# Performance work log

Hardware: AMD Instinct MI355X
Metric: run time of the kernel (lower is better)

Reference implementation:

```python
import jax, jax.numpy as jnp
import numpy as np

B, S, D, N, C = 32, 1024, 256, 32, 64
ROUTING_ITERS = 3


def setup_inputs() -> dict:
    key = jax.random.key(0)
    k1, k2 = jax.random.split(key)
    x = jax.random.normal(k1, (B, S, D), dtype=jnp.float32)
    W = jax.random.normal(k2, (N, D, C), dtype=jnp.float32) * 0.1
    return {"x": x, "W": W}


def _squash(s, eps=1e-8):
    # s: [B, N, C]; squash along last dim
    sq_norm = jnp.sum(s * s, axis=-1, keepdims=True)
    return (sq_norm / (1.0 + sq_norm)) * s / jnp.sqrt(sq_norm + eps)


def reference(x, W):
    # Prediction vectors: u_hat[b,s,n,c] = sum_d x[b,s,d] * W[n,d,c]
    u_hat = jnp.einsum('bsd,ndc->bsnc', x, W)  # [B, S, N, C]
    b_logits = jnp.zeros(u_hat.shape[:3], dtype=u_hat.dtype)  # [B, S, N]
    v = None
    for i in range(ROUTING_ITERS):
        c = jax.nn.softmax(b_logits, axis=2)               # [B, S, N]
        s = jnp.einsum('bsn,bsnc->bnc', c, u_hat)          # [B, N, C]
        v = _squash(s)                                      # [B, N, C]
        if i < ROUTING_ITERS - 1:
            agreement = jnp.einsum('bsnc,bnc->bsn', u_hat, v)
            b_logits = b_logits + agreement
    return v
```

## Files before the change

### kernel.cpp

```cpp
#include <hip/hip_runtime.h>
#include <math.h>

namespace {
constexpr int B_ = 32, S_ = 1024, D_ = 256, N_ = 32, C_ = 64;
constexpr int NC_ = N_ * C_;
constexpr int XP_ = 16;

typedef __bf16 bf16x8 __attribute__((ext_vector_type(8)));
typedef __bf16 bf16x4 __attribute__((ext_vector_type(4)));
typedef float floatx4 __attribute__((ext_vector_type(4)));

constexpr int XS_ = 264;
constexpr int TS_ = 264;
constexpr int CS_ = 72;
}

extern "C" __global__ __launch_bounds__(256) void k_stage(
    const float* __restrict__ x, float* __restrict__ xsum_part,
    __bf16* __restrict__ xb_ws) {
  const int b = blockIdx.x, sb = blockIdx.y, t = threadIdx.x;
  const float* xb = x + ((size_t)b * S_ + sb * 64) * D_;
  float a = 0.f;
  #pragma unroll 8
  for (int s = 0; s < 64; ++s) a += xb[s * D_ + t];
  xsum_part[((size_t)b * XP_ + sb) * D_ + t] = a;

  __bf16* xo = xb_ws + ((size_t)(b * XP_ + sb)) * (64 * D_);
  #pragma unroll
  for (int i = 0; i < 16; ++i) {
    int pos = i * 1024 + t * 4;
    float4 f = *(const float4*)(xb + pos);
    bf16x4 p4;
    p4[0] = (__bf16)f.x; p4[1] = (__bf16)f.y;
    p4[2] = (__bf16)f.z; p4[3] = (__bf16)f.w;
    *(bf16x4*)(xo + pos) = p4;
  }
}

extern "C" __global__ __launch_bounds__(256) void k_small(
    const float* __restrict__ z, const float* __restrict__ W,
    float* __restrict__ t_fp, __bf16* __restrict__ t_bhi,
    __bf16* __restrict__ t_blo, float* __restrict__ vout,
    float* __restrict__ yzero,
    int P, int zb, int zp, int zn, float scale, int accum, int final_) {
  __shared__ float zloc[256];
  __shared__ float sq_red[4][64];
  __shared__ float v_lds[64];
  const int b = blockIdx.x, n = blockIdx.y, t = threadIdx.x;

  float a = 0.f;
  for (int p = 0; p < P; ++p) a += z[(size_t)b * zb + (size_t)p * zp + n * zn + t];
  zloc[t] = a;
  if (yzero) yzero[((size_t)b * N_ + n) * D_ + t] = 0.f;
  __syncthreads();

  const int c = t & 63, dq = t >> 6;
  const float* Wn = W + (size_t)n * (D_ * C_);
  float s = 0.f;
  #pragma unroll 8
  for (int dd = 0; dd < 64; ++dd) {
    int d = dq * 64 + dd;
    s += zloc[d] * Wn[d * 64 + c];
  }
  sq_red[dq][c] = s;
  __syncthreads();

  if (t < 64) {
    float sc = (sq_red[0][t] + sq_red[1][t] + sq_red[2][t] + sq_red[3][t]) * scale;
    float sq = sc * sc;
    #pragma unroll
    for (int m = 1; m <= 32; m <<= 1) sq += __shfl_xor(sq, m);
    float scl = sq / ((1.f + sq) * sqrtf(sq + 1e-8f));
    float v = sc * scl;
    v_lds[t] = v;
    if (final_) vout[(size_t)b * NC_ + n * 64 + t] = v;
  }
  __syncthreads();

  if (!final_) {
    const float4* W4 = (const float4*)Wn + t * 16;
    float acc = 0.f;
    #pragma unroll
    for (int q = 0; q < 16; ++q) {
      float4 wv = W4[q];
      acc += wv.x * v_lds[q * 4] + wv.y * v_lds[q * 4 + 1] +
             wv.z * v_lds[q * 4 + 2] + wv.w * v_lds[q * 4 + 3];
    }
    size_t idx = ((size_t)b * N_ + n) * D_ + t;
    float tf = acc + (accum ? t_fp[idx] : 0.f);
    t_fp[idx] = tf;
    __bf16 hi = (__bf16)tf;
    t_bhi[idx] = hi;
    t_blo[idx] = (__bf16)(tf - (float)hi);
  }
}

extern "C" __global__ __launch_bounds__(256) void k_pass(
    const __bf16* __restrict__ xb_ws, const __bf16* __restrict__ t_bhi,
    const __bf16* __restrict__ t_blo, float* __restrict__ y) {
  __shared__ __align__(16) __bf16 x_lds[64 * XS_];
  __shared__ __align__(16) __bf16 th_lds[N_ * TS_];
  __shared__ __align__(16) __bf16 tl_lds[N_ * TS_];
  __shared__ __align__(16) __bf16 c_Th[N_ * CS_];
  __shared__ __align__(16) __bf16 c_Tl[N_ * CS_];
  const int b = blockIdx.x, ch = blockIdx.y;
  const int t = threadIdx.x, w = t >> 6, lane = t & 63;
  const int quad = lane >> 4, l16 = lane & 15;

  #pragma unroll
  for (int e = 0; e < 4; ++e) {
    int idx = e * 2048 + t * 8;
    int n = idx >> 8, d = idx & 255;
    *(uint4*)(th_lds + n * TS_ + d) = *(const uint4*)(t_bhi + (size_t)b * 8192 + idx);
    *(uint4*)(tl_lds + n * TS_ + d) = *(const uint4*)(t_blo + (size_t)b * 8192 + idx);
  }
  const __bf16* xsrc = xb_ws + ((size_t)(b * XP_ + ch)) * (64 * D_);
  #pragma unroll
  for (int e = 0; e < 8; ++e) {
    int idx = e * 2048 + t * 8;
    int row = idx >> 8, col = idx & 255;
    *(uint4*)(x_lds + row * XS_ + col) = *(const uint4*)(xsrc + idx);
  }
  __syncthreads();

  floatx4 acc[2];
  acc[0] = (floatx4){0.f, 0.f, 0.f, 0.f};
  acc[1] = (floatx4){0.f, 0.f, 0.f, 0.f};
  const int sbase = w * 16;
  #pragma unroll
  for (int k0 = 0; k0 < 256; k0 += 32) {
    int ks = k0 + quad * 8;
    bf16x8 bfrag = *(const bf16x8*)(x_lds + (sbase + l16) * XS_ + ks);
    #pragma unroll
    for (int i = 0; i < 2; ++i) {
      bf16x8 ah = *(const bf16x8*)(th_lds + (i * 16 + l16) * TS_ + ks);
      bf16x8 al = *(const bf16x8*)(tl_lds + (i * 16 + l16) * TS_ + ks);
      acc[i] = __builtin_amdgcn_mfma_f32_16x16x32_bf16(ah, bfrag, acc[i], 0, 0, 0);
      acc[i] = __builtin_amdgcn_mfma_f32_16x16x32_bf16(al, bfrag, acc[i], 0, 0, 0);
    }
  }
  float mx = -1e30f;
  #pragma unroll
  for (int i = 0; i < 2; ++i)
    #pragma unroll
    for (int r = 0; r < 4; ++r) mx = fmaxf(mx, acc[i][r]);
  mx = fmaxf(mx, __shfl_xor(mx, 16));
  mx = fmaxf(mx, __shfl_xor(mx, 32));
  float e_[2][4];
  float ss = 0.f;
  #pragma unroll
  for (int i = 0; i < 2; ++i)
    #pragma unroll
    for (int r = 0; r < 4; ++r) { e_[i][r] = __expf(acc[i][r] - mx); ss += e_[i][r]; }
  ss += __shfl_xor(ss, 16);
  ss += __shfl_xor(ss, 32);
  float inv = 1.f / ss;
  #pragma unroll
  for (int i = 0; i < 2; ++i)
    #pragma unroll
    for (int r = 0; r < 4; ++r) {
      float cv = e_[i][r] * inv;
      __bf16 chi = (__bf16)cv;
      int o = (i * 16 + quad * 4 + r) * CS_ + sbase + l16;
      c_Th[o] = chi;
      c_Tl[o] = (__bf16)(cv - (float)chi);
    }
  __syncthreads();

  floatx4 acc2[2][4];
  #pragma unroll
  for (int i = 0; i < 2; ++i)
    #pragma unroll
    for (int dt = 0; dt < 4; ++dt) acc2[i][dt] = (floatx4){0.f, 0.f, 0.f, 0.f};
  const int dbase = w * 64;
  #pragma unroll
  for (int k0 = 0; k0 < 64; k0 += 32) {
    int ks = k0 + quad * 8;
    bf16x8 ah[2], al[2];
    #pragma unroll
    for (int i = 0; i < 2; ++i) {
      ah[i] = *(const bf16x8*)(c_Th + (i * 16 + l16) * CS_ + ks);
      al[i] = *(const bf16x8*)(c_Tl + (i * 16 + l16) * CS_ + ks);
    }
    #pragma unroll
    for (int dt = 0; dt < 4; ++dt) {
      bf16x8 bfr;
      #pragma unroll
      for (int j8 = 0; j8 < 8; ++j8)
        bfr[j8] = x_lds[(ks + j8) * XS_ + dbase + dt * 16 + l16];
      #pragma unroll
      for (int i = 0; i < 2; ++i) {
        acc2[i][dt] = __builtin_amdgcn_mfma_f32_16x16x32_bf16(ah[i], bfr, acc2[i][dt], 0, 0, 0);
        acc2[i][dt] = __builtin_amdgcn_mfma_f32_16x16x32_bf16(al[i], bfr, acc2[i][dt], 0, 0, 0);
      }
    }
  }
  #pragma unroll
  for (int i = 0; i < 2; ++i)
    #pragma unroll
    for (int dt = 0; dt < 4; ++dt)
      #pragma unroll
      for (int r = 0; r < 4; ++r) {
        int n = i * 16 + quad * 4 + r;
        int d = dbase + dt * 16 + l16;
        atomicAdd(&y[((size_t)b * N_ + n) * D_ + d], acc2[i][dt][r]);
      }
}

extern "C" void kernel_launch(void* const* d_in, const int* in_sizes, int n_in,
                              void* d_out, int out_size, void* d_ws, size_t ws_size,
                              hipStream_t stream) {
  const float* x = (const float*)d_in[0];
  const float* W = (const float*)d_in[1];
  float* out = (float*)d_out;

  char* ws = (char*)d_ws;
  __bf16* xb_ws = (__bf16*)ws;
  float* xsum_part = (float*)(ws + 16777216);
  float* y1 = (float*)(ws + 16777216 + 524288);
  float* y2 = y1 + B_ * N_ * D_;
  float* t_fp = y2 + B_ * N_ * D_;
  __bf16* t_bhi = (__bf16*)(t_fp + B_ * N_ * D_);
  __bf16* t_blo = t_bhi + B_ * N_ * D_;

  k_stage<<<dim3(B_, XP_), 256, 0, stream>>>(x, xsum_part, xb_ws);

  k_small<<<dim3(B_, N_), 256, 0, stream>>>(
      xsum_part, W, t_fp, t_bhi, t_blo, nullptr, y1,
      XP_, XP_ * D_, D_, 0, 1.f / 32.f, 0, 0);

  k_pass<<<dim3(B_, XP_), 256, 0, stream>>>(xb_ws, t_bhi, t_blo, y1);

  k_small<<<dim3(B_, N_), 256, 0, stream>>>(
      y1, W, t_fp, t_bhi, t_blo, nullptr, y2,
      1, N_ * D_, 0, D_, 1.f, 1, 0);

  k_pass<<<dim3(B_, XP_), 256, 0, stream>>>(xb_ws, t_bhi, t_blo, y2);

  k_small<<<dim3(B_, N_), 256, 0, stream>>>(
      y2, W, t_fp, t_bhi, t_blo, out, nullptr,
      1, N_ * D_, 0, D_, 1.f, 0, 1);
}
```

Baseline: 158.5 us.

## Fuse all routing stages into one persistent kernel with grid barriers

```diff
diff --git a/kernel.cpp b/kernel.cpp
--- a/kernel.cpp
+++ b/kernel.cpp
@@ -5,239 +5,281 @@
 constexpr int B_ = 32, S_ = 1024, D_ = 256, N_ = 32, C_ = 64;
 constexpr int NC_ = N_ * C_;
 constexpr int XP_ = 16;
+constexpr unsigned NBLK = B_ * XP_;
 
 typedef __bf16 bf16x8 __attribute__((ext_vector_type(8)));
 typedef __bf16 bf16x4 __attribute__((ext_vector_type(4)));
 typedef float floatx4 __attribute__((ext_vector_type(4)));
 
 constexpr int XS_ = 264;
-constexpr int TS_ = 264;
 constexpr int CS_ = 72;
 }
 
-extern "C" __global__ __launch_bounds__(256) void k_stage(
-    const float* __restrict__ x, float* __restrict__ xsum_part,
-    __bf16* __restrict__ xb_ws) {
-  const int b = blockIdx.x, sb = blockIdx.y, t = threadIdx.x;
-  const float* xb = x + ((size_t)b * S_ + sb * 64) * D_;
-  float a = 0.f;
-  #pragma unroll 8
-  for (int s = 0; s < 64; ++s) a += xb[s * D_ + t];
-  xsum_part[((size_t)b * XP_ + sb) * D_ + t] = a;
-
-  __bf16* xo = xb_ws + ((size_t)(b * XP_ + sb)) * (64 * D_);
-  #pragma unroll
-  for (int i = 0; i < 16; ++i) {
-    int pos = i * 1024 + t * 4;
-    float4 f = *(const float4*)(xb + pos);
-    bf16x4 p4;
-    p4[0] = (__bf16)f.x; p4[1] = (__bf16)f.y;
-    p4[2] = (__bf16)f.z; p4[3] = (__bf16)f.w;
-    *(bf16x4*)(xo + pos) = p4;
-  }
-}
-
-extern "C" __global__ __launch_bounds__(256) void k_small(
-    const float* __restrict__ z, const float* __restrict__ W,
-    float* __restrict__ t_fp, __bf16* __restrict__ t_bhi,
-    __bf16* __restrict__ t_blo, float* __restrict__ vout,
-    float* __restrict__ yzero,
-    int P, int zb, int zp, int zn, float scale, int accum, int final_) {
-  __shared__ float zloc[256];
+__device__ __forceinline__ void gsync(unsigned* cnt, unsigned* go, unsigned e,
+                                      int t) {
+  __syncthreads();
+  if (t == 0) {
+    __threadfence();
+    unsigned a = __hip_atomic_fetch_add(cnt, 1u, __ATOMIC_ACQ_REL,
+                                        __HIP_MEMORY_SCOPE_AGENT) + 1u;
+    if (a == e * NBLK) {
+      __hip_atomic_store(go, e, __ATOMIC_RELEASE, __HIP_MEMORY_SCOPE_AGENT);
+    } else {
+      while (__hip_atomic_load(go, __ATOMIC_ACQUIRE,
+                               __HIP_MEMORY_SCOPE_AGENT) < e) {
+        __builtin_amdgcn_s_sleep(32);
+      }
+    }
+    __threadfence();
+  }
+  __syncthreads();
+}
+
+extern "C" __global__ __launch_bounds__(256, 2) void k_fused(
+    const float* __restrict__ x, const float* __restrict__ W,
+    float* __restrict__ out, float* __restrict__ xsum_part,
+    float* __restrict__ y1, float* __restrict__ y2,
+    __bf16* __restrict__ t_bhi, __bf16* __restrict__ t_blo,
+    unsigned* bar_cnt, unsigned* bar_go) {
+  __shared__ __align__(16) __bf16 x_lds[64 * XS_];
+  __shared__ __align__(16) __bf16 c_Th[N_ * CS_];
+  __shared__ __align__(16) __bf16 c_Tl[N_ * CS_];
+  __shared__ __align__(16) float scr[1024];
   __shared__ float sq_red[4][64];
   __shared__ float v_lds[64];
-  const int b = blockIdx.x, n = blockIdx.y, t = threadIdx.x;
-
-  float a = 0.f;
-  for (int p = 0; p < P; ++p) a += z[(size_t)b * zb + (size_t)p * zp + n * zn + t];
-  zloc[t] = a;
-  if (yzero) yzero[((size_t)b * N_ + n) * D_ + t] = 0.f;
+
+  const int bid = blockIdx.x;
+  const int b = bid >> 4, ch = bid & 15;
+  const int t = threadIdx.x, w = t >> 6, lane = t & 63;
+  const int quad = lane >> 4, l16 = lane & 15;
+
+  {
+    const float* xb = x + ((size_t)b * S_ + ch * 64) * D_;
+    float s0 = 0.f, s1 = 0.f, s2 = 0.f, s3 = 0.f;
+#pragma unroll
+    for (int i = 0; i < 16; ++i) {
+      int pos = i * 1024 + t * 4;
+      int row = pos >> 8, col = pos & 255;
+      float4 f = *(const float4*)(xb + pos);
+      bf16x4 p4;
+      p4[0] = (__bf16)f.x; p4[1] = (__bf16)f.y;
+      p4[2] = (__bf16)f.z; p4[3] = (__bf16)f.w;
+      *(bf16x4*)(x_lds + row * XS_ + col) = p4;
+      s0 += f.x; s1 += f.y; s2 += f.z; s3 += f.w;
+    }
+    ((float4*)scr)[t] = make_float4(s0, s1, s2, s3);
+  }
   __syncthreads();
-
-  const int c = t & 63, dq = t >> 6;
-  const float* Wn = W + (size_t)n * (D_ * C_);
-  float s = 0.f;
-  #pragma unroll 8
-  for (int dd = 0; dd < 64; ++dd) {
-    int d = dq * 64 + dd;
-    s += zloc[d] * Wn[d * 64 + c];
-  }
-  sq_red[dq][c] = s;
-  __syncthreads();
-
   if (t < 64) {
-    float sc = (sq_red[0][t] + sq_red[1][t] + sq_red[2][t] + sq_red[3][t]) * scale;
-    float sq = sc * sc;
-    #pragma unroll
-    for (int m = 1; m <= 32; m <<= 1) sq += __shfl_xor(sq, m);
-    float scl = sq / ((1.f + sq) * sqrtf(sq + 1e-8f));
-    float v = sc * scl;
-    v_lds[t] = v;
-    if (final_) vout[(size_t)b * NC_ + n * 64 + t] = v;
-  }
-  __syncthreads();
-
-  if (!final_) {
+    float4 a0 = ((float4*)scr)[t], a1 = ((float4*)scr)[t + 64],
+           a2 = ((float4*)scr)[t + 128], a3 = ((float4*)scr)[t + 192];
+    float4 r;
+    r.x = a0.x + a1.x + a2.x + a3.x;
+    r.y = a0.y + a1.y + a2.y + a3.y;
+    r.z = a0.z + a1.z + a2.z + a3.z;
+    r.w = a0.w + a1.w + a2.w + a3.w;
+    *(float4*)(xsum_part + (size_t)bid * D_ + t * 4) = r;
+  }
+
+  auto small_sv = [&](const float* zsrc, int P, int zp, const float* Wn,
+                      float scale) {
+    __syncthreads();
+    float a = 0.f;
+    for (int p = 0; p < P; ++p) a += zsrc[(size_t)p * zp + t];
+    scr[t] = a;
+    __syncthreads();
+    const int c = t & 63, dq = t >> 6;
+    float s = 0.f;
+#pragma unroll 8
+    for (int dd = 0; dd < 64; ++dd) {
+      int d = dq * 64 + dd;
+      s += scr[d] * Wn[d * 64 + c];
+    }
+    sq_red[dq][c] = s;
+    __syncthreads();
+    if (t < 64) {
+      float sc =
+          (sq_red[0][t] + sq_red[1][t] + sq_red[2][t] + sq_red[3][t]) * scale;
+      float sq = sc * sc;
+#pragma unroll
+      for (int m = 1; m <= 32; m <<= 1) sq += __shfl_xor(sq, m);
+      float scl = sq / ((1.f + sq) * sqrtf(sq + 1e-8f));
+      v_lds[t] = sc * scl;
+    }
+    __syncthreads();
+  };
+
+  auto wdotv = [&](const float* Wn) {
     const float4* W4 = (const float4*)Wn + t * 16;
     float acc = 0.f;
-    #pragma unroll
+#pragma unroll
     for (int q = 0; q < 16; ++q) {
       float4 wv = W4[q];
       acc += wv.x * v_lds[q * 4] + wv.y * v_lds[q * 4 + 1] +
              wv.z * v_lds[q * 4 + 2] + wv.w * v_lds[q * 4 + 3];
     }
+    return acc;
+  };
+
+  auto pass = [&](float* y) {
+    const __bf16* tbh = t_bhi + (size_t)b * (N_ * D_);
+    const __bf16* tbl = t_blo + (size_t)b * (N_ * D_);
+    floatx4 acc[2];
+    acc[0] = (floatx4){0.f, 0.f, 0.f, 0.f};
+    acc[1] = (floatx4){0.f, 0.f, 0.f, 0.f};
+    const int sbase = w * 16;
+#pragma unroll
+    for (int k0 = 0; k0 < 256; k0 += 32) {
+      int ks = k0 + quad * 8;
+      bf16x8 bfrag = *(const bf16x8*)(x_lds + (sbase + l16) * XS_ + ks);
+#pragma unroll
+      for (int i = 0; i < 2; ++i) {
+        bf16x8 ah = *(const bf16x8*)(tbh + (i * 16 + l16) * D_ + ks);
+        bf16x8 al = *(const bf16x8*)(tbl + (i * 16 + l16) * D_ + ks);
+        acc[i] = __builtin_amdgcn_mfma_f32_16x16x32_bf16(ah, bfrag, acc[i], 0, 0, 0);
+        acc[i] = __builtin_amdgcn_mfma_f32_16x16x32_bf16(al, bfrag, acc[i], 0, 0, 0);
+      }
+    }
+    float mx = -1e30f;
+#pragma unroll
+    for (int i = 0; i < 2; ++i)
+#pragma unroll
+      for (int r = 0; r < 4; ++r) mx = fmaxf(mx, acc[i][r]);
+    mx = fmaxf(mx, __shfl_xor(mx, 16));
+    mx = fmaxf(mx, __shfl_xor(mx, 32));
+    float e_[2][4];
+    float ss = 0.f;
+#pragma unroll
+    for (int i = 0; i < 2; ++i)
+#pragma unroll
+      for (int r = 0; r < 4; ++r) {
+        e_[i][r] = __expf(acc[i][r] - mx);
+        ss += e_[i][r];
+      }
+    ss += __shfl_xor(ss, 16);
+    ss += __shfl_xor(ss, 32);
+    float inv = 1.f / ss;
+#pragma unroll
+    for (int i = 0; i < 2; ++i)
+#pragma unroll
+      for (int r = 0; r < 4; ++r) {
+        float cv = e_[i][r] * inv;
+        __bf16 chi = (__bf16)cv;
+        int o = (i * 16 + quad * 4 + r) * CS_ + sbase + l16;
+        c_Th[o] = chi;
+        c_Tl[o] = (__bf16)(cv - (float)chi);
+      }
+    __syncthreads();
+
+    floatx4 acc2[2][4];
+#pragma unroll
+    for (int i = 0; i < 2; ++i)
+#pragma unroll
+      for (int dt = 0; dt < 4; ++dt) acc2[i][dt] = (floatx4){0.f, 0.f, 0.f, 0.f};
+    const int dbase = w * 64;
+#pragma unroll
+    for (int k0 = 0; k0 < 64; k0 += 32) {
+      int ks = k0 + quad * 8;
+      bf16x8 ah[2], al[2];
+#pragma unroll
+      for (int i = 0; i < 2; ++i) {
+        ah[i] = *(const bf16x8*)(c_Th + (i * 16 + l16) * CS_ + ks);
+        al[i] = *(const bf16x8*)(c_Tl + (i * 16 + l16) * CS_ + ks);
+      }
+#pragma unroll
+      for (int dt = 0; dt < 4; ++dt) {
+        bf16x8 bfr;
+#pragma unroll
+        for (int j8 = 0; j8 < 8; ++j8)
+          bfr[j8] = x_lds[(ks + j8) * XS_ + dbase + dt * 16 + l16];
+#pragma unroll
+        for (int i = 0; i < 2; ++i) {
+          acc2[i][dt] =
+              __builtin_amdgcn_mfma_f32_16x16x32_bf16(ah[i], bfr, acc2[i][dt], 0, 0, 0);
+          acc2[i][dt] =
+              __builtin_amdgcn_mfma_f32_16x16x32_bf16(al[i], bfr, acc2[i][dt], 0, 0, 0);
+        }
+      }
+    }
+#pragma unroll
+    for (int i = 0; i < 2; ++i)
+#pragma unroll
+      for (int dt = 0; dt < 4; ++dt)
+#pragma unroll
+        for (int r = 0; r < 4; ++r) {
+          int n = i * 16 + quad * 4 + r;
+          int d = dbase + dt * 16 + l16;
+          atomicAdd(&y[((size_t)b * N_ + n) * D_ + d], acc2[i][dt][r]);
+        }
+    __syncthreads();
+  };
+
+  float treg[2];
+
+  gsync(bar_cnt, bar_go, 1, t);
+
+#pragma unroll
+  for (int j = 0; j < 2; ++j) {
+    const int n = ch * 2 + j;
+    const float* Wn = W + (size_t)n * (D_ * C_);
+    small_sv(xsum_part + (size_t)b * XP_ * D_, XP_, D_, Wn, 1.f / 32.f);
+    float acc = wdotv(Wn);
+    treg[j] = acc;
     size_t idx = ((size_t)b * N_ + n) * D_ + t;
-    float tf = acc + (accum ? t_fp[idx] : 0.f);
-    t_fp[idx] = tf;
-    __bf16 hi = (__bf16)tf;
+    __bf16 hi = (__bf16)acc;
     t_bhi[idx] = hi;
-    t_blo[idx] = (__bf16)(tf - (float)hi);
-  }
-}
-
-extern "C" __global__ __launch_bounds__(256) void k_pass(
-    const __bf16* __restrict__ xb_ws, const __bf16* __restrict__ t_bhi,
-    const __bf16* __restrict__ t_blo, float* __restrict__ y) {
-  __shared__ __align__(16) __bf16 x_lds[64 * XS_];
-  __shared__ __align__(16) __bf16 th_lds[N_ * TS_];
-  __shared__ __align__(16) __bf16 tl_lds[N_ * TS_];
-  __shared__ __align__(16) __bf16 c_Th[N_ * CS_];
-  __shared__ __align__(16) __bf16 c_Tl[N_ * CS_];
-  const int b = blockIdx.x, ch = blockIdx.y;
-  const int t = threadIdx.x, w = t >> 6, lane = t & 63;
-  const int quad = lane >> 4, l16 = lane & 15;
-
-  #pragma unroll
-  for (int e = 0; e < 4; ++e) {
-    int idx = e * 2048 + t * 8;
-    int n = idx >> 8, d = idx & 255;
-    *(uint4*)(th_lds + n * TS_ + d) = *(const uint4*)(t_bhi + (size_t)b * 8192 + idx);
-    *(uint4*)(tl_lds + n * TS_ + d) = *(const uint4*)(t_blo + (size_t)b * 8192 + idx);
-  }
-  const __bf16* xsrc = xb_ws + ((size_t)(b * XP_ + ch)) * (64 * D_);
-  #pragma unroll
-  for (int e = 0; e < 8; ++e) {
-    int idx = e * 2048 + t * 8;
-    int row = idx >> 8, col = idx & 255;
-    *(uint4*)(x_lds + row * XS_ + col) = *(const uint4*)(xsrc + idx);
-  }
-  __syncthreads();
-
-  floatx4 acc[2];
-  acc[0] = (floatx4){0.f, 0.f, 0.f, 0.f};
-  acc[1] = (floatx4){0.f, 0.f, 0.f, 0.f};
-  const int sbase = w * 16;
-  #pragma unroll
-  for (int k0 = 0; k0 < 256; k0 += 32) {
-    int ks = k0 + quad * 8;
-    bf16x8 bfrag = *(const bf16x8*)(x_lds + (sbase + l16) * XS_ + ks);
-    #pragma unroll
-    for (int i = 0; i < 2; ++i) {
-      bf16x8 ah = *(const bf16x8*)(th_lds + (i * 16 + l16) * TS_ + ks);
-      bf16x8 al = *(const bf16x8*)(tl_lds + (i * 16 + l16) * TS_ + ks);
-      acc[i] = __builtin_amdgcn_mfma_f32_16x16x32_bf16(ah, bfrag, acc[i], 0, 0, 0);
-      acc[i] = __builtin_amdgcn_mfma_f32_16x16x32_bf16(al, bfrag, acc[i], 0, 0, 0);
-    }
-  }
-  float mx = -1e30f;
-  #pragma unroll
-  for (int i = 0; i < 2; ++i)
-    #pragma unroll
-    for (int r = 0; r < 4; ++r) mx = fmaxf(mx, acc[i][r]);
-  mx = fmaxf(mx, __shfl_xor(mx, 16));
-  mx = fmaxf(mx, __shfl_xor(mx, 32));
-  float e_[2][4];
-  float ss = 0.f;
-  #pragma unroll
-  for (int i = 0; i < 2; ++i)
-    #pragma unroll
-    for (int r = 0; r < 4; ++r) { e_[i][r] = __expf(acc[i][r] - mx); ss += e_[i][r]; }
-  ss += __shfl_xor(ss, 16);
-  ss += __shfl_xor(ss, 32);
-  float inv = 1.f / ss;
-  #pragma unroll
-  for (int i = 0; i < 2; ++i)
-    #pragma unroll
-    for (int r = 0; r < 4; ++r) {
-      float cv = e_[i][r] * inv;
-      __bf16 chi = (__bf16)cv;
-      int o = (i * 16 + quad * 4 + r) * CS_ + sbase + l16;
-      c_Th[o] = chi;
-      c_Tl[o] = (__bf16)(cv - (float)chi);
-    }
-  __syncthreads();
-
-  floatx4 acc2[2][4];
-  #pragma unroll
-  for (int i = 0; i < 2; ++i)
-    #pragma unroll
-    for (int dt = 0; dt < 4; ++dt) acc2[i][dt] = (floatx4){0.f, 0.f, 0.f, 0.f};
-  const int dbase = w * 64;
-  #pragma unroll
-  for (int k0 = 0; k0 < 64; k0 += 32) {
-    int ks = k0 + quad * 8;
-    bf16x8 ah[2], al[2];
-    #pragma unroll
-    for (int i = 0; i < 2; ++i) {
-      ah[i] = *(const bf16x8*)(c_Th + (i * 16 + l16) * CS_ + ks);
-      al[i] = *(const bf16x8*)(c_Tl + (i * 16 + l16) * CS_ + ks);
-    }
-    #pragma unroll
-    for (int dt = 0; dt < 4; ++dt) {
-      bf16x8 bfr;
-      #pragma unroll
-      for (int j8 = 0; j8 < 8; ++j8)
-        bfr[j8] = x_lds[(ks + j8) * XS_ + dbase + dt * 16 + l16];
-      #pragma unroll
-      for (int i = 0; i < 2; ++i) {
-        acc2[i][dt] = __builtin_amdgcn_mfma_f32_16x16x32_bf16(ah[i], bfr, acc2[i][dt], 0, 0, 0);
-        acc2[i][dt] = __builtin_amdgcn_mfma_f32_16x16x32_bf16(al[i], bfr, acc2[i][dt], 0, 0, 0);
-      }
-    }
-  }
-  #pragma unroll
-  for (int i = 0; i < 2; ++i)
-    #pragma unroll
-    for (int dt = 0; dt < 4; ++dt)
-      #pragma unroll
-      for (int r = 0; r < 4; ++r) {
-        int n = i * 16 + quad * 4 + r;
-        int d = dbase + dt * 16 + l16;
-        atomicAdd(&y[((size_t)b * N_ + n) * D_ + d], acc2[i][dt][r]);
-      }
+    t_blo[idx] = (__bf16)(acc - (float)hi);
+    y1[idx] = 0.f;
+  }
+
+  gsync(bar_cnt, bar_go, 2, t);
+  pass(y1);
+  gsync(bar_cnt, bar_go, 3, t);
+
+#pragma unroll
+  for (int j = 0; j < 2; ++j) {
+    const int n = ch * 2 + j;
+    const float* Wn = W + (size_t)n * (D_ * C_);
+    small_sv(y1 + ((size_t)b * N_ + n) * D_, 1, 0, Wn, 1.f);
+    float acc = treg[j] + wdotv(Wn);
+    treg[j] = acc;
+    size_t idx = ((size_t)b * N_ + n) * D_ + t;
+    __bf16 hi = (__bf16)acc;
+    t_bhi[idx] = hi;
+    t_blo[idx] = (__bf16)(acc - (float)hi);
+    y2[idx] = 0.f;
+  }
+
+  gsync(bar_cnt, bar_go, 4, t);
+  pass(y2);
+  gsync(bar_cnt, bar_go, 5, t);
+
+#pragma unroll
+  for (int j = 0; j < 2; ++j) {
+    const int n = ch * 2 + j;
+    const float* Wn = W + (size_t)n * (D_ * C_);
+    small_sv(y2 + ((size_t)b * N_ + n) * D_, 1, 0, Wn, 1.f);
+    if (t < 64) out[(size_t)b * NC_ + n * 64 + t] = v_lds[t];
+  }
 }
 
 extern "C" void kernel_launch(void* const* d_in, const int* in_sizes, int n_in,
-                              void* d_out, int out_size, void* d_ws, size_t ws_size,
-                              hipStream_t stream) {
+                              void* d_out, int out_size, void* d_ws,
+                              size_t ws_size, hipStream_t stream) {
   const float* x = (const float*)d_in[0];
   const float* W = (const float*)d_in[1];
   float* out = (float*)d_out;
 
   char* ws = (char*)d_ws;
-  __bf16* xb_ws = (__bf16*)ws;
-  float* xsum_part = (float*)(ws + 16777216);
-  float* y1 = (float*)(ws + 16777216 + 524288);
+  float* xsum_part = (float*)ws;
+  float* y1 = (float*)(ws + 524288);
   float* y2 = y1 + B_ * N_ * D_;
-  float* t_fp = y2 + B_ * N_ * D_;
-  __bf16* t_bhi = (__bf16*)(t_fp + B_ * N_ * D_);
+  __bf16* t_bhi = (__bf16*)(y2 + B_ * N_ * D_);
   __bf16* t_blo = t_bhi + B_ * N_ * D_;
-
-  k_stage<<<dim3(B_, XP_), 256, 0, stream>>>(x, xsum_part, xb_ws);
-
-  k_small<<<dim3(B_, N_), 256, 0, stream>>>(
-      xsum_part, W, t_fp, t_bhi, t_blo, nullptr, y1,
-      XP_, XP_ * D_, D_, 0, 1.f / 32.f, 0, 0);
-
-  k_pass<<<dim3(B_, XP_), 256, 0, stream>>>(xb_ws, t_bhi, t_blo, y1);
-
-  k_small<<<dim3(B_, N_), 256, 0, stream>>>(
-      y1, W, t_fp, t_bhi, t_blo, nullptr, y2,
-      1, N_ * D_, 0, D_, 1.f, 1, 0);
-
-  k_pass<<<dim3(B_, XP_), 256, 0, stream>>>(xb_ws, t_bhi, t_blo, y2);
-
-  k_small<<<dim3(B_, N_), 256, 0, stream>>>(
-      y2, W, t_fp, t_bhi, t_blo, out, nullptr,
-      1, N_ * D_, 0, D_, 1.f, 0, 1);
-}
+  unsigned* bar = (unsigned*)(ws + 3670016);
+
+  hipMemsetAsync(bar, 0, 256, stream);
+
+  k_fused<<<dim3(NBLK), dim3(256), 0, stream>>>(x, W, out, xsum_part, y1, y2,
+                                                t_bhi, t_blo, bar, bar + 32);
+}
```

Measured after the change: 329.1 us. +107.6%, slower.

## Read fp32 x directly in pass kernels and replace atomics with partial sums

Applied to the files above, without the earlier changes.

```diff
diff --git a/kernel.cpp b/kernel.cpp
--- a/kernel.cpp
+++ b/kernel.cpp
@@ -16,32 +16,19 @@
 }
 
 extern "C" __global__ __launch_bounds__(256) void k_stage(
-    const float* __restrict__ x, float* __restrict__ xsum_part,
-    __bf16* __restrict__ xb_ws) {
+    const float* __restrict__ x, float* __restrict__ xsum_part) {
   const int b = blockIdx.x, sb = blockIdx.y, t = threadIdx.x;
   const float* xb = x + ((size_t)b * S_ + sb * 64) * D_;
   float a = 0.f;
   #pragma unroll 8
   for (int s = 0; s < 64; ++s) a += xb[s * D_ + t];
   xsum_part[((size_t)b * XP_ + sb) * D_ + t] = a;
-
-  __bf16* xo = xb_ws + ((size_t)(b * XP_ + sb)) * (64 * D_);
-  #pragma unroll
-  for (int i = 0; i < 16; ++i) {
-    int pos = i * 1024 + t * 4;
-    float4 f = *(const float4*)(xb + pos);
-    bf16x4 p4;
-    p4[0] = (__bf16)f.x; p4[1] = (__bf16)f.y;
-    p4[2] = (__bf16)f.z; p4[3] = (__bf16)f.w;
-    *(bf16x4*)(xo + pos) = p4;
-  }
 }
 
 extern "C" __global__ __launch_bounds__(256) void k_small(
     const float* __restrict__ z, const float* __restrict__ W,
     float* __restrict__ t_fp, __bf16* __restrict__ t_bhi,
     __bf16* __restrict__ t_blo, float* __restrict__ vout,
-    float* __restrict__ yzero,
     int P, int zb, int zp, int zn, float scale, int accum, int final_) {
   __shared__ float zloc[256];
   __shared__ float sq_red[4][64];
@@ -51,7 +38,6 @@
   float a = 0.f;
   for (int p = 0; p < P; ++p) a += z[(size_t)b * zb + (size_t)p * zp + n * zn + t];
   zloc[t] = a;
-  if (yzero) yzero[((size_t)b * N_ + n) * D_ + t] = 0.f;
   __syncthreads();
 
   const int c = t & 63, dq = t >> 6;
@@ -96,8 +82,8 @@
 }
 
 extern "C" __global__ __launch_bounds__(256) void k_pass(
-    const __bf16* __restrict__ xb_ws, const __bf16* __restrict__ t_bhi,
-    const __bf16* __restrict__ t_blo, float* __restrict__ y) {
+    const float* __restrict__ x, const __bf16* __restrict__ t_bhi,
+    const __bf16* __restrict__ t_blo, float* __restrict__ y_part) {
   __shared__ __align__(16) __bf16 x_lds[64 * XS_];
   __shared__ __align__(16) __bf16 th_lds[N_ * TS_];
   __shared__ __align__(16) __bf16 tl_lds[N_ * TS_];
@@ -114,12 +100,16 @@
     *(uint4*)(th_lds + n * TS_ + d) = *(const uint4*)(t_bhi + (size_t)b * 8192 + idx);
     *(uint4*)(tl_lds + n * TS_ + d) = *(const uint4*)(t_blo + (size_t)b * 8192 + idx);
   }
-  const __bf16* xsrc = xb_ws + ((size_t)(b * XP_ + ch)) * (64 * D_);
-  #pragma unroll
-  for (int e = 0; e < 8; ++e) {
-    int idx = e * 2048 + t * 8;
+  const float* xsrc = x + ((size_t)b * S_ + ch * 64) * D_;
+  #pragma unroll
+  for (int e = 0; e < 16; ++e) {
+    int idx = e * 1024 + t * 4;
     int row = idx >> 8, col = idx & 255;
-    *(uint4*)(x_lds + row * XS_ + col) = *(const uint4*)(xsrc + idx);
+    float4 f = *(const float4*)(xsrc + idx);
+    bf16x4 p4;
+    p4[0] = (__bf16)f.x; p4[1] = (__bf16)f.y;
+    p4[2] = (__bf16)f.z; p4[3] = (__bf16)f.w;
+    *(bf16x4*)(x_lds + row * XS_ + col) = p4;
   }
   __syncthreads();
 
@@ -195,6 +185,7 @@
       }
     }
   }
+  float* yo = y_part + ((size_t)(b * XP_ + ch) * N_) * D_;
   #pragma unroll
   for (int i = 0; i < 2; ++i)
     #pragma unroll
@@ -203,7 +194,7 @@
       for (int r = 0; r < 4; ++r) {
         int n = i * 16 + quad * 4 + r;
         int d = dbase + dt * 16 + l16;
-        atomicAdd(&y[((size_t)b * N_ + n) * D_ + d], acc2[i][dt][r]);
+        yo[n * D_ + d] = acc2[i][dt][r];
       }
 }
 
@@ -215,29 +206,27 @@
   float* out = (float*)d_out;
 
   char* ws = (char*)d_ws;
-  __bf16* xb_ws = (__bf16*)ws;
-  float* xsum_part = (float*)(ws + 16777216);
-  float* y1 = (float*)(ws + 16777216 + 524288);
-  float* y2 = y1 + B_ * N_ * D_;
-  float* t_fp = y2 + B_ * N_ * D_;
+  float* xsum_part = (float*)ws;
+  float* y_part = (float*)(ws + 524288);
+  float* t_fp = (float*)(ws + 524288 + 16777216);
   __bf16* t_bhi = (__bf16*)(t_fp + B_ * N_ * D_);
   __bf16* t_blo = t_bhi + B_ * N_ * D_;
 
-  k_stage<<<dim3(B_, XP_), 256, 0, stream>>>(x, xsum_part, xb_ws);
+  k_stage<<<dim3(B_, XP_), 256, 0, stream>>>(x, xsum_part);
 
   k_small<<<dim3(B_, N_), 256, 0, stream>>>(
-      xsum_part, W, t_fp, t_bhi, t_blo, nullptr, y1,
+      xsum_part, W, t_fp, t_bhi, t_blo, nullptr,
       XP_, XP_ * D_, D_, 0, 1.f / 32.f, 0, 0);
 
-  k_pass<<<dim3(B_, XP_), 256, 0, stream>>>(xb_ws, t_bhi, t_blo, y1);
+  k_pass<<<dim3(B_, XP_), 256, 0, stream>>>(x, t_bhi, t_blo, y_part);
 
   k_small<<<dim3(B_, N_), 256, 0, stream>>>(
-      y1, W, t_fp, t_bhi, t_blo, nullptr, y2,
-      1, N_ * D_, 0, D_, 1.f, 1, 0);
-
-  k_pass<<<dim3(B_, XP_), 256, 0, stream>>>(xb_ws, t_bhi, t_blo, y2);
+      y_part, W, t_fp, t_bhi, t_blo, nullptr,
+      XP_, XP_ * N_ * D_, N_ * D_, D_, 1.f, 1, 0);
+
+  k_pass<<<dim3(B_, XP_), 256, 0, stream>>>(x, t_bhi, t_blo, y_part);
 
   k_small<<<dim3(B_, N_), 256, 0, stream>>>(
-      y2, W, t_fp, t_bhi, t_blo, out, nullptr,
-      1, N_ * D_, 0, D_, 1.f, 0, 1);
-}
+      y_part, W, t_fp, t_bhi, t_blo, out,
+      XP_, XP_ * N_ * D_, N_ * D_, D_, 1.f, 0, 1);
+}
```

After: 159.0 us. Within noise of the previous version (+0.3%).
